# Kernel tuning notes

Hardware: AMD Instinct MI355X
Metric: run time of the kernel (lower is better)

## Reference

```python
import jax, jax.numpy as jnp
import numpy as np

N, E, F_IN, H, G, K = 50000, 800000, 64, 200, 256, 3


def setup_inputs() -> dict:
    key = jax.random.key(0)
    ks = jax.random.split(key, 12)
    x = jax.random.normal(ks[0], (N, F_IN), jnp.float32)
    edge_index = jax.random.randint(ks[1], (2, E), 0, N, dtype=jnp.int64)
    batch = jnp.sort(jax.random.randint(ks[2], (N,), 0, G, dtype=jnp.int64))
    lmax = 1.5 + jax.random.uniform(ks[3], (G,), jnp.float32)  # per-graph lambda_max

    def lin(k, i, o):
        return (jax.random.normal(k, (K, i, o), jnp.float32) / np.sqrt(i)).astype(jnp.float32)

    return dict(
        x=x, edge_index=edge_index, batch=batch, lmax=lmax,
        W1=lin(ks[4], F_IN, H), b1=jnp.zeros((H,), jnp.float32),
        W2=lin(ks[5], H, H),    b2=jnp.zeros((H,), jnp.float32),
        W3=lin(ks[6], H, H),    b3=jnp.zeros((H,), jnp.float32),
        W4=lin(ks[7], H, H),    b4=jnp.zeros((H,), jnp.float32),
        fc_w=(jax.random.normal(ks[8], (2 * H, 2), jnp.float32) / np.sqrt(2 * H)).astype(jnp.float32),
        fc_b=jnp.zeros((2,), jnp.float32),
    )


def reference(x, edge_index, batch, lmax, W1, b1, W2, b2, W3, b3, W4, b4, fc_w, fc_b):
    n = x.shape[0]
    g = lmax.shape[0]
    src, dst = edge_index[0], edge_index[1]

    # PyG ChebConv sym normalization: L_hat = 2/lambda_max * (I - D^-1/2 A D^-1/2) - I
    deg = jax.ops.segment_sum(jnp.ones(src.shape[0], x.dtype), src, num_segments=n)
    dis = jnp.where(deg > 0, jnp.maximum(deg, 1.0) ** -0.5, 0.0)  # deg^{-1/2}, inf -> 0
    scale = 2.0 / lmax                                            # [G]
    w = -dis[src] * dis[dst] * scale[batch[src]]                  # off-diagonal edge weights [E]
    diag = scale[batch] - 1.0                                     # diagonal of L_hat, [N]

    def prop(h):  # L_hat @ h via sparse scatter
        return jax.ops.segment_sum(w[:, None] * h[src], dst, num_segments=n) + diag[:, None] * h

    def cheb(h, W, b):  # K=3 Chebyshev recurrence
        Tx0 = h
        Tx1 = prop(h)
        Tx2 = 2.0 * prop(Tx1) - Tx0
        return Tx0 @ W[0] + Tx1 @ W[1] + Tx2 @ W[2] + b

    h = jax.nn.relu(cheb(x, W1, b1))
    h = jax.nn.relu(cheb(h, W2, b2))
    h = jax.nn.relu(cheb(h, W3, b3))
    h = jax.nn.relu(cheb(h, W4, b4))

    cnt = jax.ops.segment_sum(jnp.ones(n, h.dtype), batch, num_segments=g)
    pooled_mean = jax.ops.segment_sum(h, batch, num_segments=g) / jnp.maximum(cnt, 1.0)[:, None]
    pooled_max = jax.ops.segment_max(h, batch, num_segments=g)
    z = jnp.concatenate([pooled_mean, pooled_max], axis=1) @ fc_w + fc_b
    return jax.nn.log_softmax(z, axis=1)
```

## Files before the change

### kernel.cpp

```cpp
#include <hip/hip_runtime.h>
#include <math.h>

#define NN 50000
#define MP 50048
#define NE 800000
#define FIN 64
#define HD 200
#define NG 256
#define SCAN_B 256
#define KPAD 224
#define NT 13

typedef _Float16 h16;
typedef __attribute__((ext_vector_type(8))) _Float16 half8;
typedef __attribute__((ext_vector_type(4))) float float4v;
typedef unsigned long long u64;

__global__ void k_deg(const int* __restrict__ src, const int* __restrict__ dst,
                      float* __restrict__ deg, int* __restrict__ cnt_dst, int E) {
    int e = blockIdx.x * blockDim.x + threadIdx.x;
    if (e < E) {
        atomicAdd(&deg[src[e]], 1.0f);
        atomicAdd(&cnt_dst[dst[e]], 1);
    }
}

__global__ void k_node_prep(float* __restrict__ degdis, const int* __restrict__ batch,
                            const float* __restrict__ lmax, float* __restrict__ diag, int n) {
    int i = blockIdx.x * blockDim.x + threadIdx.x;
    if (i < n) {
        float d = degdis[i];
        degdis[i] = (d > 0.f) ? (1.0f / sqrtf(fmaxf(d, 1.0f))) : 0.0f;
        diag[i] = 2.0f / lmax[batch[i]] - 1.0f;
    }
}

__global__ void k_scan1(const int* __restrict__ cnt, int* __restrict__ excl,
                        int* __restrict__ bsum, int n) {
    __shared__ int sh[SCAN_B];
    int tid = threadIdx.x;
    int i = blockIdx.x * SCAN_B + tid;
    int v = (i < n) ? cnt[i] : 0;
    sh[tid] = v;
    __syncthreads();
    for (int off = 1; off < SCAN_B; off <<= 1) {
        int t = (tid >= off) ? sh[tid - off] : 0;
        __syncthreads();
        sh[tid] += t;
        __syncthreads();
    }
    if (i < n) excl[i] = sh[tid] - v;
    if (tid == SCAN_B - 1) bsum[blockIdx.x] = sh[tid];
}

__global__ void k_scan2(int* __restrict__ bsum, int nb) {
    __shared__ int sh[SCAN_B];
    int tid = threadIdx.x;
    int v = (tid < nb) ? bsum[tid] : 0;
    sh[tid] = v;
    __syncthreads();
    for (int off = 1; off < SCAN_B; off <<= 1) {
        int t = (tid >= off) ? sh[tid - off] : 0;
        __syncthreads();
        sh[tid] += t;
        __syncthreads();
    }
    if (tid < nb) bsum[tid] = sh[tid] - v;
}

__global__ void k_scan3(int* __restrict__ excl, const int* __restrict__ bsum, int n) {
    int i = blockIdx.x * SCAN_B + threadIdx.x;
    if (i < n) excl[i] += bsum[blockIdx.x];
}

__global__ void k_fillcsr(const int* __restrict__ src, const int* __restrict__ dst,
                          const int* __restrict__ batch, const float* __restrict__ lmax,
                          const float* __restrict__ dis, const int* __restrict__ rowstart,
                          int* __restrict__ fill, u64* __restrict__ csr, int E) {
    int e = blockIdx.x * blockDim.x + threadIdx.x;
    if (e < E) {
        int s = src[e], d = dst[e];
        int pos = rowstart[d] + atomicAdd(&fill[d], 1);
        float w = -dis[s] * dis[d] * (2.0f / lmax[batch[s]]);
        csr[pos] = (unsigned)s | ((u64)__float_as_uint(w) << 32);
    }
}

__global__ void k_split(const float* __restrict__ x, h16* __restrict__ x16, int total) {
    int i = blockIdx.x * blockDim.x + threadIdx.x;
    if (i < total) x16[i] = (h16)x[i];
}

__global__ void k_wprep(const float* __restrict__ W, h16* __restrict__ out,
                        int fin, int ksteps, int total) {
    int idx = blockIdx.x * blockDim.x + threadIdx.x;
    if (idx >= total) return;
    int kk = idx & 31;
    int r = idx >> 5;
    int nn = r % 208;
    int r2 = r / 208;
    int ks = r2 % ksteps;
    int seg = r2 / ksteps;
    int k = ks * 32 + kk;
    out[idx] = (nn < HD && k < fin) ? (h16)W[((size_t)seg * fin + k) * HD + nn] : (h16)0.f;
}

__global__ void k_bounds(const int* __restrict__ batch, int* __restrict__ gstart, int n) {
    int g = blockIdx.x * blockDim.x + threadIdx.x;
    if (g > NG) return;
    if (g == NG) { gstart[NG] = n; return; }
    int lo = 0, hi = n;
    while (lo < hi) {
        int mid = (lo + hi) >> 1;
        if (batch[mid] < g) lo = mid + 1; else hi = mid;
    }
    gstart[g] = lo;
}

__global__ __launch_bounds__(256) void k_gather(
    const int* __restrict__ rowstart, const int* __restrict__ rowcnt,
    const u64* __restrict__ csr, const float* __restrict__ diag,
    const h16* __restrict__ hin16, const h16* __restrict__ h016,
    h16* __restrict__ hout16, int s16, int lsh, int n, int mode) {
    int per = 256 >> lsh;
    int i = blockIdx.x * per + (threadIdx.x >> lsh);
    if (i >= n) return;
    int lane = threadIdx.x & ((1 << lsh) - 1);
    int c0 = lane * 4;
    if (c0 >= s16) return;
    int start = rowstart[i], cnt = rowcnt[i];
    float a0 = 0.f, a1 = 0.f, a2 = 0.f, a3 = 0.f;
    union U { uint2 u; h16 h[4]; };
    const u64* cp = csr + start;
    int k = 0;
    for (; k + 7 < cnt; k += 8) {
        u64 e[8];
#pragma unroll
        for (int j = 0; j < 8; ++j) e[j] = cp[k + j];
        U p[8];
#pragma unroll
        for (int j = 0; j < 8; ++j)
            p[j].u = *(const uint2*)(hin16 + (size_t)(unsigned)(e[j] & 0xffffffffu) * s16 + c0);
#pragma unroll
        for (int j = 0; j < 8; ++j) {
            float w = __uint_as_float((unsigned)(e[j] >> 32));
            a0 += w * (float)p[j].h[0];
            a1 += w * (float)p[j].h[1];
            a2 += w * (float)p[j].h[2];
            a3 += w * (float)p[j].h[3];
        }
    }
    for (; k + 1 < cnt; k += 2) {
        u64 e0 = cp[k], e1 = cp[k + 1];
        U p0, p1;
        p0.u = *(const uint2*)(hin16 + (size_t)(unsigned)(e0 & 0xffffffffu) * s16 + c0);
        p1.u = *(const uint2*)(hin16 + (size_t)(unsigned)(e1 & 0xffffffffu) * s16 + c0);
        float w0 = __uint_as_float((unsigned)(e0 >> 32));
        float w1 = __uint_as_float((unsigned)(e1 >> 32));
        a0 += w0 * (float)p0.h[0] + w1 * (float)p1.h[0];
        a1 += w0 * (float)p0.h[1] + w1 * (float)p1.h[1];
        a2 += w0 * (float)p0.h[2] + w1 * (float)p1.h[2];
        a3 += w0 * (float)p0.h[3] + w1 * (float)p1.h[3];
    }
    if (k < cnt) {
        u64 e0 = cp[k];
        U p0;
        p0.u = *(const uint2*)(hin16 + (size_t)(unsigned)(e0 & 0xffffffffu) * s16 + c0);
        float w0 = __uint_as_float((unsigned)(e0 >> 32));
        a0 += w0 * (float)p0.h[0];
        a1 += w0 * (float)p0.h[1];
        a2 += w0 * (float)p0.h[2];
        a3 += w0 * (float)p0.h[3];
    }
    float dg = diag[i];
    U hs; hs.u = *(const uint2*)(hin16 + (size_t)i * s16 + c0);
    float v0 = a0 + dg * (float)hs.h[0];
    float v1 = a1 + dg * (float)hs.h[1];
    float v2 = a2 + dg * (float)hs.h[2];
    float v3 = a3 + dg * (float)hs.h[3];
    if (mode == 1) {
        U h0; h0.u = *(const uint2*)(h016 + (size_t)i * s16 + c0);
        v0 = 2.f * v0 - (float)h0.h[0];
        v1 = 2.f * v1 - (float)h0.h[1];
        v2 = 2.f * v2 - (float)h0.h[2];
        v3 = 2.f * v3 - (float)h0.h[3];
    }
    U o;
    o.h[0] = (h16)v0; o.h[1] = (h16)v1; o.h[2] = (h16)v2; o.h[3] = (h16)v3;
    *(uint2*)(hout16 + (size_t)i * s16 + c0) = o.u;
}

__global__ __launch_bounds__(256) void k_gemm16(
    const h16* __restrict__ A0, const h16* __restrict__ A1, const h16* __restrict__ A2,
    int strideA, int ksteps,
    const h16* __restrict__ Wt, const float* __restrict__ bias,
    float* __restrict__ outF, h16* __restrict__ out16, int n) {
    int tid = threadIdx.x;
    int wave = tid >> 6, lane = tid & 63;
    int nq = lane & 15, quad = lane >> 4;
    int row0 = (blockIdx.x * 4 + wave) * 32;
    const h16* Aseg[3] = {A0, A1, A2};

    float4v acc[2][NT];
#pragma unroll
    for (int r = 0; r < 2; r++)
#pragma unroll
        for (int t = 0; t < NT; t++) acc[r][t] = (float4v)0.f;

    for (int seg = 0; seg < 3; ++seg) {
        const h16* Ab = Aseg[seg] + (size_t)(row0 + nq) * strideA + quad * 8;
        const h16* Bb = Wt + (size_t)seg * ksteps * 208 * 32 + (size_t)nq * 32 + quad * 8;
        for (int ks = 0; ks < ksteps; ++ks) {
            half8 af0 = *(const half8*)(Ab + ks * 32);
            half8 af1 = *(const half8*)(Ab + 16 * strideA + ks * 32);
            const h16* Bk = Bb + (size_t)ks * 208 * 32;
#pragma unroll
            for (int t = 0; t < NT; ++t) {
                half8 bf = *(const half8*)(Bk + t * 16 * 32);
                acc[0][t] = __builtin_amdgcn_mfma_f32_16x16x32_f16(af0, bf, acc[0][t], 0, 0, 0);
                acc[1][t] = __builtin_amdgcn_mfma_f32_16x16x32_f16(af1, bf, acc[1][t], 0, 0, 0);
            }
        }
    }
#pragma unroll
    for (int r = 0; r < 2; ++r) {
        int rowb = row0 + r * 16 + quad * 4;
#pragma unroll
        for (int t = 0; t < NT; ++t) {
            int col = t * 16 + nq;
            if (col >= HD) continue;
            float bj = bias[col];
#pragma unroll
            for (int g = 0; g < 4; ++g) {
                int row = rowb + g;
                if (row < n) {
                    float v = fmaxf(acc[r][t][g] + bj, 0.0f);
                    if (outF)  outF[(size_t)row * HD + col] = v;
                    if (out16) out16[(size_t)row * KPAD + col] = (h16)v;
                }
            }
        }
    }
}

__global__ __launch_bounds__(256) void k_pool_fc(
    const float* __restrict__ Hf, const int* __restrict__ gstart,
    const float* __restrict__ fcw, const float* __restrict__ fcb,
    float* __restrict__ out) {
    __shared__ float red[8];
    int g = blockIdx.x;
    int j = threadIdx.x;
    int i0 = gstart[g], i1 = gstart[g + 1];
    float s0 = 0.f, s1 = 0.f, s2 = 0.f, s3 = 0.f, mx = 0.f;
    if (j < HD) {
        int i = i0;
        for (; i + 3 < i1; i += 4) {
            float v0 = Hf[(size_t)i * HD + j];
            float v1 = Hf[(size_t)(i + 1) * HD + j];
            float v2 = Hf[(size_t)(i + 2) * HD + j];
            float v3 = Hf[(size_t)(i + 3) * HD + j];
            s0 += v0; s1 += v1; s2 += v2; s3 += v3;
            mx = fmaxf(mx, fmaxf(fmaxf(v0, v1), fmaxf(v2, v3)));
        }
        for (; i < i1; ++i) {
            float v = Hf[(size_t)i * HD + j];
            s0 += v; mx = fmaxf(mx, v);
        }
    }
    float cntf = (float)(i1 - i0);
    float mean = (s0 + s1 + s2 + s3) / fmaxf(cntf, 1.f);
    float p0 = 0.f, p1 = 0.f;
    if (j < HD) {
        p0 = mean * fcw[2 * j]     + mx * fcw[2 * (HD + j)];
        p1 = mean * fcw[2 * j + 1] + mx * fcw[2 * (HD + j) + 1];
    }
#pragma unroll
    for (int o = 32; o > 0; o >>= 1) {
        p0 += __shfl_down(p0, o);
        p1 += __shfl_down(p1, o);
    }
    int wave = j >> 6, lane = j & 63;
    if (lane == 0) { red[wave * 2] = p0; red[wave * 2 + 1] = p1; }
    __syncthreads();
    if (j == 0) {
        float z0 = red[0] + red[2] + red[4] + red[6] + fcb[0];
        float z1 = red[1] + red[3] + red[5] + red[7] + fcb[1];
        float m = fmaxf(z0, z1);
        float lse = m + logf(expf(z0 - m) + expf(z1 - m));
        out[g * 2 + 0] = z0 - lse;
        out[g * 2 + 1] = z1 - lse;
    }
}

extern "C" void kernel_launch(void* const* d_in, const int* in_sizes, int n_in,
                              void* d_out, int out_size, void* d_ws, size_t ws_size,
                              hipStream_t stream) {
    const float* x     = (const float*)d_in[0];
    const int*   edge  = (const int*)d_in[1];
    const int*   batch = (const int*)d_in[2];
    const float* lmax  = (const float*)d_in[3];
    const float* W1 = (const float*)d_in[4];  const float* b1 = (const float*)d_in[5];
    const float* W2 = (const float*)d_in[6];  const float* b2 = (const float*)d_in[7];
    const float* W3 = (const float*)d_in[8];  const float* b3 = (const float*)d_in[9];
    const float* W4 = (const float*)d_in[10]; const float* b4 = (const float*)d_in[11];
    const float* fcw = (const float*)d_in[12]; const float* fcb = (const float*)d_in[13];
    float* out = (float*)d_out;

    const int n = NN, E = NE;
    const int* src = edge;
    const int* dst = edge + E;

    float* ws = (float*)d_ws;
    size_t off = 0;
    auto alloc = [&](size_t nfloats) { float* p = ws + off; off += (nfloats + 3) & ~(size_t)3; return p; };
    float* dis    = alloc(NN);
    float* diag   = alloc(NN);
    int*   cntd   = (int*)alloc(NN);
    int*   rowst  = (int*)alloc(NN);
    int*   fill   = (int*)alloc(NN);
    int*   bsum   = (int*)alloc(SCAN_B);
    u64*   csr    = (u64*)alloc((size_t)NE * 2);
    int*   gstart = (int*)alloc(NG + 1);
    float* H      = alloc((size_t)MP * HD);
    h16*   x16    = (h16*)alloc((size_t)MP * FIN / 2);
    h16*   hi0    = (h16*)alloc((size_t)MP * KPAD / 2);
    h16*   hi1    = (h16*)alloc((size_t)MP * KPAD / 2);
    h16*   hi2    = (h16*)alloc((size_t)MP * KPAD / 2);
    const int WSZ0 = 3 * 2 * 208 * 32;
    const int WSZ  = 3 * 7 * 208 * 32;
    h16* wt0 = (h16*)alloc(WSZ0 / 2);
    h16* wt1 = (h16*)alloc(WSZ / 2);
    h16* wt2 = (h16*)alloc(WSZ / 2);
    h16* wt3 = (h16*)alloc(WSZ / 2);

    dim3 blk(256);
    int gE = (E + 255) / 256;
    int gN = (n + 255) / 256;
    int gScan = (n + SCAN_B - 1) / SCAN_B;
    int gGemm = MP / 128;

    k_wprep<<<(WSZ0 + 255) / 256, blk, 0, stream>>>(W1, wt0, FIN, 2, WSZ0);
    k_wprep<<<(WSZ + 255) / 256, blk, 0, stream>>>(W2, wt1, HD, 7, WSZ);
    k_wprep<<<(WSZ + 255) / 256, blk, 0, stream>>>(W3, wt2, HD, 7, WSZ);
    k_wprep<<<(WSZ + 255) / 256, blk, 0, stream>>>(W4, wt3, HD, 7, WSZ);
    k_split<<<(NN * FIN + 255) / 256, blk, 0, stream>>>(x, x16, NN * FIN);
    k_bounds<<<2, blk, 0, stream>>>(batch, gstart, n);
    hipMemsetAsync(hi0, 0, (size_t)MP * KPAD * 2, stream);

    hipMemsetAsync(dis, 0, (size_t)NN * 4, stream);
    hipMemsetAsync(cntd, 0, (size_t)NN * 4, stream);
    hipMemsetAsync(fill, 0, (size_t)NN * 4, stream);
    k_deg<<<gE, blk, 0, stream>>>(src, dst, dis, cntd, E);
    k_node_prep<<<gN, blk, 0, stream>>>(dis, batch, lmax, diag, n);
    k_scan1<<<gScan, blk, 0, stream>>>(cntd, rowst, bsum, n);
    k_scan2<<<1, blk, 0, stream>>>(bsum, gScan);
    k_scan3<<<gScan, blk, 0, stream>>>(rowst, bsum, n);
    k_fillcsr<<<gE, blk, 0, stream>>>(src, dst, batch, lmax, dis, rowst, fill, csr, E);

    const h16* wt[4] = {wt0, wt1, wt2, wt3};
    const float* bl[4] = {b1, b2, b3, b4};
    for (int l = 0; l < 4; l++) {
        int s16 = (l == 0) ? FIN : KPAD;
        int lsh = (l == 0) ? 4 : 6;
        int per = 256 >> lsh;
        int gGat = (n + per - 1) / per;
        int ksteps = (l == 0) ? 2 : 7;
        const h16* a0 = (l == 0) ? x16 : hi0;
        k_gather<<<gGat, blk, 0, stream>>>(rowst, cntd, csr, diag, a0, a0, hi1, s16, lsh, n, 0);
        k_gather<<<gGat, blk, 0, stream>>>(rowst, cntd, csr, diag, hi1, a0, hi2, s16, lsh, n, 1);
        k_gemm16<<<gGemm, blk, 0, stream>>>(a0, hi1, hi2, s16, ksteps, wt[l], bl[l],
                                            (l == 3) ? H : nullptr,
                                            (l < 3) ? hi0 : nullptr, n);
    }

    k_pool_fc<<<NG, blk, 0, stream>>>(H, gstart, fcw, fcb, out);
}
```

Measured before the change: 884.3 us.

## Replace global atomic degree counting with shared-memory packed histograms plus reduction

Computes source-degree and destination-count arrays with per-block shared-memory histograms that pack two 16-bit counters per word, processed in two node-range passes, then sums the 256 block partials in a separate reduce kernel. This removes the global atomics on degree and count arrays and the memsets that preceded them. In exchange it writes and rereads a large partial-histogram buffer and adds extra launches.

```diff
diff --git a/kernel.cpp b/kernel.cpp
--- a/kernel.cpp
+++ b/kernel.cpp
@@ -10,27 +10,62 @@
 #define SCAN_B 256
 #define KPAD 224
 #define NT 13
+#define HB 12544
+#define PER_B 3125
 
 typedef _Float16 h16;
 typedef __attribute__((ext_vector_type(8))) _Float16 half8;
 typedef __attribute__((ext_vector_type(4))) float float4v;
 typedef unsigned long long u64;
 
-__global__ void k_deg(const int* __restrict__ src, const int* __restrict__ dst,
-                      float* __restrict__ deg, int* __restrict__ cnt_dst, int E) {
-    int e = blockIdx.x * blockDim.x + threadIdx.x;
-    if (e < E) {
-        atomicAdd(&deg[src[e]], 1.0f);
-        atomicAdd(&cnt_dst[dst[e]], 1);
-    }
-}
-
-__global__ void k_node_prep(float* __restrict__ degdis, const int* __restrict__ batch,
-                            const float* __restrict__ lmax, float* __restrict__ diag, int n) {
+__global__ __launch_bounds__(256) void k_hist(const int* __restrict__ idx,
+                                              unsigned* __restrict__ partial, int E) {
+    __shared__ unsigned h[HB];
+    int tid = threadIdx.x;
+    int e0 = blockIdx.x * PER_B;
+    int v[13];
+#pragma unroll
+    for (int j = 0; j < 13; ++j) {
+        int o = j * 256 + tid;
+        v[j] = (o < PER_B) ? idx[e0 + o] : -1;
+    }
+#pragma unroll
+    for (int pass = 0; pass < 2; ++pass) {
+        for (int t = tid; t < HB; t += 256) h[t] = 0;
+        __syncthreads();
+        int lo = pass * (2 * HB);
+#pragma unroll
+        for (int j = 0; j < 13; ++j) {
+            int vv = v[j] - lo;
+            if (vv >= 0 && vv < 2 * HB)
+                atomicAdd(&h[vv >> 1], (vv & 1) ? 0x10000u : 1u);
+        }
+        __syncthreads();
+        unsigned* pb = partial + ((size_t)pass * 256 + blockIdx.x) * HB;
+        for (int t = tid; t < HB; t += 256) pb[t] = h[t];
+        __syncthreads();
+    }
+}
+
+__global__ void k_hreduce(const unsigned* __restrict__ partial, int* __restrict__ cnt, int n) {
+    int i = blockIdx.x * blockDim.x + threadIdx.x;
+    if (i >= 2 * HB) return;
+    int pass = i / HB, p = i - pass * HB;
+    const unsigned* pb = partial + (size_t)pass * 256 * HB + p;
+    unsigned s = 0;
+    for (int b = 0; b < 256; ++b) s += pb[(size_t)b * HB];
+    int n0 = pass * 2 * HB + 2 * p;
+    if (n0 < n)     cnt[n0]     = (int)(s & 0xffffu);
+    if (n0 + 1 < n) cnt[n0 + 1] = (int)(s >> 16);
+}
+
+__global__ void k_node_prep(const int* __restrict__ degi, const int* __restrict__ batch,
+                            const float* __restrict__ lmax, float* __restrict__ dis,
+                            float* __restrict__ diag, int n) {
     int i = blockIdx.x * blockDim.x + threadIdx.x;
     if (i < n) {
-        float d = degdis[i];
-        degdis[i] = (d > 0.f) ? (1.0f / sqrtf(fmaxf(d, 1.0f))) : 0.0f;
+        int d = degi[i];
+        dis[i] = (d > 0) ? (1.0f / sqrtf((float)d)) : 0.0f;
         diag[i] = 2.0f / lmax[batch[i]] - 1.0f;
     }
 }
@@ -313,6 +348,7 @@
     float* ws = (float*)d_ws;
     size_t off = 0;
     auto alloc = [&](size_t nfloats) { float* p = ws + off; off += (nfloats + 3) & ~(size_t)3; return p; };
+    int*   degi   = (int*)alloc(NN);
     float* dis    = alloc(NN);
     float* diag   = alloc(NN);
     int*   cntd   = (int*)alloc(NN);
@@ -321,6 +357,7 @@
     int*   bsum   = (int*)alloc(SCAN_B);
     u64*   csr    = (u64*)alloc((size_t)NE * 2);
     int*   gstart = (int*)alloc(NG + 1);
+    unsigned* hpart = (unsigned*)alloc((size_t)2 * 256 * HB);
     float* H      = alloc((size_t)MP * HD);
     h16*   x16    = (h16*)alloc((size_t)MP * FIN / 2);
     h16*   hi0    = (h16*)alloc((size_t)MP * KPAD / 2);
@@ -338,6 +375,7 @@
     int gN = (n + 255) / 256;
     int gScan = (n + SCAN_B - 1) / SCAN_B;
     int gGemm = MP / 128;
+    int gHR = (2 * HB + 255) / 256;
 
     k_wprep<<<(WSZ0 + 255) / 256, blk, 0, stream>>>(W1, wt0, FIN, 2, WSZ0);
     k_wprep<<<(WSZ + 255) / 256, blk, 0, stream>>>(W2, wt1, HD, 7, WSZ);
@@ -347,11 +385,13 @@
     k_bounds<<<2, blk, 0, stream>>>(batch, gstart, n);
     hipMemsetAsync(hi0, 0, (size_t)MP * KPAD * 2, stream);
 
-    hipMemsetAsync(dis, 0, (size_t)NN * 4, stream);
-    hipMemsetAsync(cntd, 0, (size_t)NN * 4, stream);
+    k_hist<<<256, blk, 0, stream>>>(src, hpart, E);
+    k_hreduce<<<gHR, blk, 0, stream>>>(hpart, degi, n);
+    k_hist<<<256, blk, 0, stream>>>(dst, hpart, E);
+    k_hreduce<<<gHR, blk, 0, stream>>>(hpart, cntd, n);
+    k_node_prep<<<gN, blk, 0, stream>>>(degi, batch, lmax, dis, diag, n);
+
     hipMemsetAsync(fill, 0, (size_t)NN * 4, stream);
-    k_deg<<<gE, blk, 0, stream>>>(src, dst, dis, cntd, E);
-    k_node_prep<<<gN, blk, 0, stream>>>(dis, batch, lmax, diag, n);
     k_scan1<<<gScan, blk, 0, stream>>>(cntd, rowst, bsum, n);
     k_scan2<<<1, blk, 0, stream>>>(bsum, gScan);
     k_scan3<<<gScan, blk, 0, stream>>>(rowst, bsum, n);
```

Measured after the change: 851.5 us. 1.04x faster.
